# Kernel tuning notes

Hardware: AMD Instinct MI355X
Metric: run time of the kernel (lower is better)

Reference implementation:

```python
import jax, jax.numpy as jnp
import numpy as np

B, S, D_MODEL, D_K = 4, 4096, 1024, 128
NEG = jnp.float32(-1e30)  # acts as -inf for masking; exp underflows to exactly 0 in fp32


def setup_inputs() -> dict:
    key = jax.random.key(0)
    ks = jax.random.split(key, 8)
    sc = 1.0 / np.sqrt(D_MODEL)
    x = jax.random.normal(ks[0], (B, S, D_MODEL), jnp.float32)
    padding_mask = (jax.random.uniform(ks[1], (B, S)) > 0.05).astype(jnp.float32)
    Wq = jax.random.normal(ks[2], (D_MODEL, D_K), jnp.float32) * sc
    bq = jax.random.normal(ks[3], (D_K,), jnp.float32) * 0.01
    Wk = jax.random.normal(ks[4], (D_MODEL, D_K), jnp.float32) * sc
    bk = jax.random.normal(ks[5], (D_K,), jnp.float32) * 0.01
    Wv = jax.random.normal(ks[6], (D_MODEL, D_K), jnp.float32) * sc
    bv = jax.random.normal(ks[7], (D_K,), jnp.float32) * 0.01
    return {"x": x, "padding_mask": padding_mask, "Wq": Wq, "bq": bq,
            "Wk": Wk, "bk": bk, "Wv": Wv, "bv": bv}


def reference(x, padding_mask, Wq, bq, Wk, bk, Wv, bv):
    # Self-attention path (enc_dec_layer_input is None), masked=True (causal).
    scale = jnp.sqrt(jnp.float32(Wq.shape[-1]))
    Q = x @ Wq + bq  # [B,S,Dk]
    K = x @ Wk + bk
    V = x @ Wv + bv
    scores = jnp.einsum('bqd,bkd->bqk', Q, K) / scale  # [B,S,S]
    # causal mask (torch: triu(1) filled with -inf) AND padding outer-product mask
    causal = jnp.tril(jnp.ones((S, S), dtype=bool))  # True = allowed
    pm = (padding_mask[:, :, None] * padding_mask[:, None, :]) > 0  # [B,S,S]
    allowed = causal[None] & pm
    scores = jnp.where(allowed, scores, NEG)
    attn = jax.nn.softmax(scores, axis=-1)
    # torch: fully-masked query rows give NaN -> nan_to_num -> 0.
    # A query row is dead iff its own token is padded (diagonal is causally allowed).
    row_alive = padding_mask > 0  # [B,S]
    attn = jnp.where(row_alive[:, :, None], attn, 0.0)
    out = jnp.einsum('bqk,bkd->bqd', attn, V)  # [B,S,Dk]
    return out
```

## Files before the change

kernel.cpp:

```cpp
#include <hip/hip_runtime.h>
#include <hip/hip_bf16.h>
#include <cstdint>

typedef __bf16 bf16x8 __attribute__((ext_vector_type(8)));
typedef float f32x4 __attribute__((ext_vector_type(4)));

#define MFMA16(a, b, c) __builtin_amdgcn_mfma_f32_16x16x32_bf16((a), (b), (c), 0, 0, 0)

__device__ __forceinline__ unsigned short f2bf(float f) {
  union { float f; unsigned u; } v; v.f = f;
  unsigned u = v.u;
  u += 0x7fffu + ((u >> 16) & 1u);
  return (unsigned short)(u >> 16);
}
__device__ __forceinline__ unsigned pk2(float a, float b) {
  __hip_bfloat162 h = __float22bfloat162_rn(make_float2(a, b));
  union { __hip_bfloat162 h; unsigned u; } v; v.h = h; return v.u;
}

__global__ __launch_bounds__(256) void convert_w(
    const float* __restrict__ Wq, const float* __restrict__ Wk,
    const float* __restrict__ Wv, unsigned short* __restrict__ wt) {
  int idx = blockIdx.x * 256 + threadIdx.x;
  int m = idx >> 17;
  int rem = idx & 131071;
  int k = rem >> 7;
  int n = rem & 127;
  const float* W = (m == 0) ? Wq : (m == 1) ? Wk : Wv;
  wt[(size_t)m * 131072 + (size_t)n * 1024 + k] = f2bf(W[(size_t)k * 128 + n]);
}

__global__ __launch_bounds__(256) void qkv_gemm(
    const float* __restrict__ x, const unsigned short* __restrict__ wt_all,
    const float* __restrict__ bq, const float* __restrict__ bk,
    const float* __restrict__ bv,
    unsigned short* __restrict__ Qg, unsigned short* __restrict__ Kg,
    unsigned short* __restrict__ Vtg) {
  __shared__ unsigned short x_lds[128][40];
  __shared__ unsigned short w_lds[128][40];
  const int tid = threadIdx.x;
  const int lane = tid & 63;
  const int w = tid >> 6;
  const int mode = blockIdx.y;
  const int m0 = blockIdx.x * 128;
  const unsigned short* wt = wt_all + (size_t)mode * 131072;
  const float* bias = (mode == 0) ? bq : (mode == 1) ? bk : bv;

  const int wr = (w >> 1) * 64;
  const int wc = (w & 1) * 64;
  const int lr = lane & 15;
  const int lk = (lane >> 4) * 8;

  f32x4 acc[4][4];
#pragma unroll
  for (int m = 0; m < 4; ++m)
#pragma unroll
    for (int n = 0; n < 4; ++n) acc[m][n] = (f32x4){0.f, 0.f, 0.f, 0.f};

  const int srow = tid >> 1;
  const int shalf = (tid & 1) * 16;
  const float* xrow = x + (size_t)(m0 + srow) * 1024 + shalf;
  const unsigned short* wrow = wt + (size_t)srow * 1024 + shalf;

  float4 xa, xb, xc, xd; uint4 wv0, wv1;
  {
    const float4* s4 = (const float4*)xrow;
    xa = s4[0]; xb = s4[1]; xc = s4[2]; xd = s4[3];
    const uint4* ws4 = (const uint4*)wrow;
    wv0 = ws4[0]; wv1 = ws4[1];
  }

  for (int k0 = 0; k0 < 1024; k0 += 32) {
    __syncthreads();
    {
      uint4 w0, w1;
      w0.x = pk2(xa.x, xa.y);  w0.y = pk2(xa.z, xa.w);
      w0.z = pk2(xb.x, xb.y);  w0.w = pk2(xb.z, xb.w);
      w1.x = pk2(xc.x, xc.y);  w1.y = pk2(xc.z, xc.w);
      w1.z = pk2(xd.x, xd.y);  w1.w = pk2(xd.z, xd.w);
      *(uint4*)&x_lds[srow][shalf] = w0;
      *(uint4*)&x_lds[srow][shalf + 8] = w1;
      *(uint4*)&w_lds[srow][shalf] = wv0;
      *(uint4*)&w_lds[srow][shalf + 8] = wv1;
    }
    __syncthreads();
    if (k0 + 32 < 1024) {
      const float4* s4 = (const float4*)(xrow + k0 + 32);
      xa = s4[0]; xb = s4[1]; xc = s4[2]; xd = s4[3];
      const uint4* ws4 = (const uint4*)(wrow + k0 + 32);
      wv0 = ws4[0]; wv1 = ws4[1];
    }
    bf16x8 af[4], bfr[4];
#pragma unroll
    for (int m = 0; m < 4; ++m) af[m] = *(const bf16x8*)&x_lds[wr + m * 16 + lr][lk];
#pragma unroll
    for (int n = 0; n < 4; ++n) bfr[n] = *(const bf16x8*)&w_lds[wc + n * 16 + lr][lk];
#pragma unroll
    for (int m = 0; m < 4; ++m)
#pragma unroll
      for (int n = 0; n < 4; ++n) acc[m][n] = MFMA16(af[m], bfr[n], acc[m][n]);
  }

  float bcol[4];
#pragma unroll
  for (int n = 0; n < 4; ++n) bcol[n] = bias[wc + n * 16 + lr];
#pragma unroll
  for (int m = 0; m < 4; ++m)
#pragma unroll
    for (int n = 0; n < 4; ++n)
#pragma unroll
      for (int r = 0; r < 4; ++r) {
        int grow = m0 + wr + m * 16 + (lane >> 4) * 4 + r;
        int col = wc + n * 16 + lr;
        float val = acc[m][n][r] + bcol[n];
        if (mode == 0) {
          val *= 0.08838834764831845f;
          Qg[(size_t)grow * 128 + col] = f2bf(val);
        } else if (mode == 1) {
          Kg[(size_t)grow * 128 + col] = f2bf(val);
        } else {
          int bb = grow >> 12, s = grow & 4095;
          Vtg[((size_t)bb * 128 + col) * 4096 + s] = f2bf(val);
        }
      }
}

struct AttnLds {
  unsigned short K_lds[64][136];
  unsigned short V_lds[128][72];
  unsigned short P_lds[4][16][68];
};

__device__ __forceinline__ void attn_tiles(
    AttnLds& S, const unsigned short* __restrict__ Kg,
    const unsigned short* __restrict__ Vtg, const float* __restrict__ pmask,
    int b, int q0, int tstart, int tend,
    const bf16x8 (&qf)[4], float& mrow, float& lsum, f32x4 (&o)[8]) {
  const int tid = threadIdx.x;
  const int lane = tid & 63;
  const int w = tid >> 6;
  const int lr = lane & 15;
  const int lg = lane >> 4;
  const int lk = lg * 8;
  const int q_own = q0 + w * 16 + lr;

  for (int t = tstart; t < tend; ++t) {
    const int k0 = t * 64;
    __syncthreads();
    {
      int kr = tid >> 2, seg = (tid & 3) * 32;
      const uint4* src = (const uint4*)(Kg + ((size_t)b * 4096 + k0 + kr) * 128 + seg);
      uint4 v0 = src[0], v1 = src[1], v2 = src[2], v3 = src[3];
      uint4* dst = (uint4*)&S.K_lds[kr][seg];
      dst[0] = v0; dst[1] = v1; dst[2] = v2; dst[3] = v3;
      int d = tid >> 1, half = (tid & 1) * 32;
      const uint4* vs = (const uint4*)(Vtg + ((size_t)b * 128 + d) * 4096 + k0 + half);
      uint4 u0 = vs[0], u1 = vs[1], u2 = vs[2], u3 = vs[3];
      uint4* vdst = (uint4*)&S.V_lds[d][half];
      vdst[0] = u0; vdst[1] = u1; vdst[2] = u2; vdst[3] = u3;
    }
    __syncthreads();

    f32x4 st[4];
#pragma unroll
    for (int f = 0; f < 4; ++f) {
      st[f] = (f32x4){0.f, 0.f, 0.f, 0.f};
#pragma unroll
      for (int dc = 0; dc < 4; ++dc) {
        bf16x8 kf = *(const bf16x8*)&S.K_lds[f * 16 + lr][dc * 32 + lk];
        st[f] = MFMA16(kf, qf[dc], st[f]);
      }
    }

    const unsigned long long mb = __ballot(pmask[(size_t)b * 4096 + k0 + lane] > 0.f);
    unsigned nib[4];
#pragma unroll
    for (int f = 0; f < 4; ++f) nib[f] = (unsigned)(mb >> (16 * f + 4 * lg)) & 0xFu;

    float mx = -1e30f;
    if (k0 + 63 > q0 + (w << 4)) {
#pragma unroll
      for (int f = 0; f < 4; ++f)
#pragma unroll
        for (int r = 0; r < 4; ++r) {
          const bool ok = (((nib[f] >> r) & 1u) != 0u) &&
                          (k0 + 16 * f + 4 * lg + r <= q_own);
          const float s = ok ? st[f][r] : -1e30f;
          st[f][r] = s;
          mx = fmaxf(mx, s);
        }
    } else {
#pragma unroll
      for (int f = 0; f < 4; ++f)
#pragma unroll
        for (int r = 0; r < 4; ++r) {
          const bool ok = ((nib[f] >> r) & 1u) != 0u;
          const float s = ok ? st[f][r] : -1e30f;
          st[f][r] = s;
          mx = fmaxf(mx, s);
        }
    }
    mx = fmaxf(mx, __shfl_xor(mx, 16));
    mx = fmaxf(mx, __shfl_xor(mx, 32));
    const float mnew = fmaxf(mrow, mx);
    const float alpha = __expf(mrow - mnew);
    mrow = mnew;

    float sum = 0.f;
#pragma unroll
    for (int f = 0; f < 4; ++f) {
      const float p0 = (st[f][0] < -1e29f) ? 0.f : __expf(st[f][0] - mnew);
      const float p1 = (st[f][1] < -1e29f) ? 0.f : __expf(st[f][1] - mnew);
      const float p2 = (st[f][2] < -1e29f) ? 0.f : __expf(st[f][2] - mnew);
      const float p3 = (st[f][3] < -1e29f) ? 0.f : __expf(st[f][3] - mnew);
      sum += (p0 + p1) + (p2 + p3);
      uint2 u; u.x = pk2(p0, p1); u.y = pk2(p2, p3);
      *(uint2*)&S.P_lds[w][lr][16 * f + 4 * lg] = u;
    }
    sum += __shfl_xor(sum, 16);
    sum += __shfl_xor(sum, 32);
    lsum = lsum * alpha + sum;
#pragma unroll
    for (int n = 0; n < 8; ++n) o[n] *= alpha;

    __asm__ volatile("s_waitcnt lgkmcnt(0)" ::: "memory");
#pragma unroll
    for (int kc = 0; kc < 2; ++kc) {
      bf16x8 pa = *(const bf16x8*)&S.P_lds[w][lr][kc * 32 + lk];
#pragma unroll
      for (int n = 0; n < 8; ++n) {
        bf16x8 vf = *(const bf16x8*)&S.V_lds[n * 16 + lr][kc * 32 + lk];
        o[n] = MFMA16(vf, pa, o[n]);
      }
    }
  }
}

__global__ __launch_bounds__(256) void attn_fwd(
    const unsigned short* __restrict__ Qg, const unsigned short* __restrict__ Kg,
    const unsigned short* __restrict__ Vtg, const float* __restrict__ pmask,
    float* __restrict__ out) {
  __shared__ AttnLds S;
  const int tid = threadIdx.x;
  const int lane = tid & 63;
  const int w = tid >> 6;
  const int b = blockIdx.y;
  const int q0 = blockIdx.x * 64;
  const int lr = lane & 15;
  const int lg = lane >> 4;
  const int lk = lg * 8;

  bf16x8 qf[4];
  {
    const unsigned short* qp = Qg + ((size_t)b * 4096 + q0 + w * 16 + lr) * 128;
#pragma unroll
    for (int dc = 0; dc < 4; ++dc) qf[dc] = *(const bf16x8*)(qp + dc * 32 + lk);
  }
  float mrow = -1e30f, lsum = 0.f;
  f32x4 o[8];
#pragma unroll
  for (int n = 0; n < 8; ++n) o[n] = (f32x4){0.f, 0.f, 0.f, 0.f};

  attn_tiles(S, Kg, Vtg, pmask, b, q0, 0, (q0 >> 6) + 1, qf, mrow, lsum, o);

  const int qrow = q0 + w * 16 + lr;
  const bool alive = pmask[(size_t)b * 4096 + qrow] > 0.f;
  const float inv = (alive && lsum > 0.f) ? 1.f / lsum : 0.f;
  float* op = out + ((size_t)b * 4096 + qrow) * 128 + 4 * lg;
#pragma unroll
  for (int n = 0; n < 8; ++n) {
    f32x4 v = o[n] * inv;
    *(f32x4*)(op + n * 16) = v;
  }
}

__global__ __launch_bounds__(256) void attn_split(
    const unsigned short* __restrict__ Qg, const unsigned short* __restrict__ Kg,
    const unsigned short* __restrict__ Vtg, const float* __restrict__ pmask,
    float* __restrict__ out, unsigned short* __restrict__ o_part,
    float* __restrict__ ml_part) {
  __shared__ AttnLds S;
  const int tid = threadIdx.x;
  const int lane = tid & 63;
  const int w = tid >> 6;
  const int L = blockIdx.x;
  const int xcd = L & 7;
  const int b = xcd >> 1;
  const int s = ((L >> 3) << 1) | (xcd & 1);
  int qb, c, nch;
  if (s < 13)       { qb = s;                 c = 0;       nch = 1; }
  else if (s < 39)  { int t = s - 13;  qb = 13 + (t >> 1); c = t & 1;  nch = 2; }
  else if (s < 78)  { int t = s - 39;  qb = 26 + t / 3;    c = t % 3;  nch = 3; }
  else if (s < 130) { int t = s - 78;  qb = 39 + (t >> 2); c = t & 3;  nch = 4; }
  else              { int t = s - 130; qb = 52 + t / 5;    c = t % 5;  nch = 5; }
  const int q0 = qb * 64;
  const int tstart = c * 13;
  const int tend = min(c * 13 + 13, qb + 1);
  const int lr = lane & 15;
  const int lg = lane >> 4;
  const int lk = lg * 8;

  bf16x8 qf[4];
  {
    const unsigned short* qp = Qg + ((size_t)b * 4096 + q0 + w * 16 + lr) * 128;
#pragma unroll
    for (int dc = 0; dc < 4; ++dc) qf[dc] = *(const bf16x8*)(qp + dc * 32 + lk);
  }
  float mrow = -1e30f, lsum = 0.f;
  f32x4 o[8];
#pragma unroll
  for (int n = 0; n < 8; ++n) o[n] = (f32x4){0.f, 0.f, 0.f, 0.f};

  attn_tiles(S, Kg, Vtg, pmask, b, q0, tstart, tend, qf, mrow, lsum, o);

  if (nch == 1) {
    const int qrow = q0 + w * 16 + lr;
    const bool alive = pmask[(size_t)b * 4096 + qrow] > 0.f;
    const float inv = (alive && lsum > 0.f) ? 1.f / lsum : 0.f;
    float* op = out + ((size_t)b * 4096 + qrow) * 128 + 4 * lg;
#pragma unroll
    for (int n = 0; n < 8; ++n) {
      f32x4 v = o[n] * inv;
      *(f32x4*)(op + n * 16) = v;
    }
  } else {
    const int slot = (b * 64 + qb) * 5 + c;
    unsigned short* op = o_part + ((size_t)slot * 64 + w * 16 + lr) * 128 + 4 * lg;
#pragma unroll
    for (int n = 0; n < 8; ++n) {
      uint2 u; u.x = pk2(o[n][0], o[n][1]); u.y = pk2(o[n][2], o[n][3]);
      *(uint2*)(op + n * 16) = u;
    }
    if (lane < 16) {
      float* mp = ml_part + ((size_t)slot * 64 + w * 16 + lane) * 2;
      mp[0] = mrow;
      mp[1] = lsum;
    }
  }
}

__global__ __launch_bounds__(256) void attn_combine(
    const unsigned short* __restrict__ o_part, const float* __restrict__ ml_part,
    const float* __restrict__ pmask, float* __restrict__ out) {
  const int tid = threadIdx.x;
  const int lane = tid & 63;
  const int w = tid >> 6;
  const int g = blockIdx.x * 4 + w;
  const int b = g / 3264;
  const int rem = g % 3264;
  const int qb = 13 + (rem >> 6);
  const int row = rem & 63;
  const int qrow = qb * 64 + row;
  const int nch = (qb + 13) / 13;
  const int pbase = (b * 64 + qb) * 5;

  float m[5], l[5];
  float M = -1e30f;
  for (int c = 0; c < nch; ++c) {
    const float* mp = ml_part + ((size_t)(pbase + c) * 64 + row) * 2;
    m[c] = mp[0];
    l[c] = mp[1];
    M = fmaxf(M, m[c]);
  }
  float L = 0.f, wgt[5];
  for (int c = 0; c < nch; ++c) {
    wgt[c] = __expf(m[c] - M);
    L += wgt[c] * l[c];
  }
  float2 acc = {0.f, 0.f};
  for (int c = 0; c < nch; ++c) {
    const unsigned u = *(const unsigned*)(o_part + ((size_t)(pbase + c) * 64 + row) * 128 + lane * 2);
    acc.x += wgt[c] * __uint_as_float(u << 16);
    acc.y += wgt[c] * __uint_as_float(u & 0xffff0000u);
  }
  const bool alive = pmask[(size_t)b * 4096 + qrow] > 0.f;
  const float inv = (alive && L > 0.f) ? 1.f / L : 0.f;
  float2* op = (float2*)(out + ((size_t)b * 4096 + qrow) * 128);
  op[lane] = make_float2(acc.x * inv, acc.y * inv);
}

extern "C" void kernel_launch(void* const* d_in, const int* in_sizes, int n_in,
                              void* d_out, int out_size, void* d_ws, size_t ws_size,
                              hipStream_t stream) {
  (void)in_sizes; (void)n_in; (void)out_size;
  const float* x  = (const float*)d_in[0];
  const float* pm = (const float*)d_in[1];
  const float* Wq = (const float*)d_in[2];
  const float* bq = (const float*)d_in[3];
  const float* Wk = (const float*)d_in[4];
  const float* bk = (const float*)d_in[5];
  const float* Wv = (const float*)d_in[6];
  const float* bv = (const float*)d_in[7];
  float* out = (float*)d_out;

  unsigned short* ws  = (unsigned short*)d_ws;
  unsigned short* wt  = ws;
  unsigned short* Qg  = ws + 393216;
  unsigned short* Kg  = Qg + 2097152;
  unsigned short* Vtg = Kg + 2097152;
  unsigned short* o_part = ws + 6684672;
  float* ml_part = (float*)(ws + 17170432);
  const size_t WS_NEED = 34996224u;

  convert_w<<<1536, 256, 0, stream>>>(Wq, Wk, Wv, wt);
  qkv_gemm<<<dim3(128, 3), 256, 0, stream>>>(x, wt, bq, bk, bv, Qg, Kg, Vtg);
  if (ws_size >= WS_NEED) {
    attn_split<<<760, 256, 0, stream>>>(Qg, Kg, Vtg, pm, out, o_part, ml_part);
    attn_combine<<<3264, 256, 0, stream>>>(o_part, ml_part, pm, out);
  } else {
    attn_fwd<<<dim3(64, 4), 256, 0, stream>>>(Qg, Kg, Vtg, pm, out);
  }
}
```

Measured before the change: 115.6 us.

## Read V directly from global, shrink split chunks to 8 tiles, raise occupancy

After: 183.0 us. +58.2%, slower.

```diff
diff --git a/kernel.cpp b/kernel.cpp
--- a/kernel.cpp
+++ b/kernel.cpp
@@ -127,14 +127,13 @@
 
 struct AttnLds {
   unsigned short K_lds[64][136];
-  unsigned short V_lds[128][72];
   unsigned short P_lds[4][16][68];
 };
 
 __device__ __forceinline__ void attn_tiles(
-    AttnLds& S, const unsigned short* __restrict__ Kg,
-    const unsigned short* __restrict__ Vtg, const float* __restrict__ pmask,
-    int b, int q0, int tstart, int tend,
+    AttnLds& S, const unsigned short* __restrict__ Kb,
+    const unsigned short* __restrict__ Vb, const float* __restrict__ pmb,
+    int q0, int tstart, int tend,
     const bf16x8 (&qf)[4], float& mrow, float& lsum, f32x4 (&o)[8]) {
   const int tid = threadIdx.x;
   const int lane = tid & 63;
@@ -149,15 +148,10 @@
     __syncthreads();
     {
       int kr = tid >> 2, seg = (tid & 3) * 32;
-      const uint4* src = (const uint4*)(Kg + ((size_t)b * 4096 + k0 + kr) * 128 + seg);
+      const uint4* src = (const uint4*)(Kb + (size_t)(k0 + kr) * 128 + seg);
       uint4 v0 = src[0], v1 = src[1], v2 = src[2], v3 = src[3];
       uint4* dst = (uint4*)&S.K_lds[kr][seg];
       dst[0] = v0; dst[1] = v1; dst[2] = v2; dst[3] = v3;
-      int d = tid >> 1, half = (tid & 1) * 32;
-      const uint4* vs = (const uint4*)(Vtg + ((size_t)b * 128 + d) * 4096 + k0 + half);
-      uint4 u0 = vs[0], u1 = vs[1], u2 = vs[2], u3 = vs[3];
-      uint4* vdst = (uint4*)&S.V_lds[d][half];
-      vdst[0] = u0; vdst[1] = u1; vdst[2] = u2; vdst[3] = u3;
     }
     __syncthreads();
 
@@ -172,7 +166,7 @@
       }
     }
 
-    const unsigned long long mb = __ballot(pmask[(size_t)b * 4096 + k0 + lane] > 0.f);
+    const unsigned long long mb = __ballot(pmb[k0 + lane] > 0.f);
     unsigned nib[4];
 #pragma unroll
     for (int f = 0; f < 4; ++f) nib[f] = (unsigned)(mb >> (16 * f + 4 * lg)) & 0xFu;
@@ -229,14 +223,14 @@
       bf16x8 pa = *(const bf16x8*)&S.P_lds[w][lr][kc * 32 + lk];
 #pragma unroll
       for (int n = 0; n < 8; ++n) {
-        bf16x8 vf = *(const bf16x8*)&S.V_lds[n * 16 + lr][kc * 32 + lk];
+        bf16x8 vf = *(const bf16x8*)(Vb + (size_t)(n * 16 + lr) * 4096 + k0 + kc * 32 + lk);
         o[n] = MFMA16(vf, pa, o[n]);
       }
     }
   }
 }
 
-__global__ __launch_bounds__(256) void attn_fwd(
+__global__ __launch_bounds__(256, 5) void attn_fwd(
     const unsigned short* __restrict__ Qg, const unsigned short* __restrict__ Kg,
     const unsigned short* __restrict__ Vtg, const float* __restrict__ pmask,
     float* __restrict__ out) {
@@ -261,7 +255,8 @@
 #pragma unroll
   for (int n = 0; n < 8; ++n) o[n] = (f32x4){0.f, 0.f, 0.f, 0.f};
 
-  attn_tiles(S, Kg, Vtg, pmask, b, q0, 0, (q0 >> 6) + 1, qf, mrow, lsum, o);
+  attn_tiles(S, Kg + (size_t)b * 4096 * 128, Vtg + (size_t)b * 128 * 4096,
+             pmask + (size_t)b * 4096, q0, 0, (q0 >> 6) + 1, qf, mrow, lsum, o);
 
   const int qrow = q0 + w * 16 + lr;
   const bool alive = pmask[(size_t)b * 4096 + qrow] > 0.f;
@@ -274,7 +269,7 @@
   }
 }
 
-__global__ __launch_bounds__(256) void attn_split(
+__global__ __launch_bounds__(256, 5) void attn_split(
     const unsigned short* __restrict__ Qg, const unsigned short* __restrict__ Kg,
     const unsigned short* __restrict__ Vtg, const float* __restrict__ pmask,
     float* __restrict__ out, unsigned short* __restrict__ o_part,
@@ -288,14 +283,22 @@
   const int b = xcd >> 1;
   const int s = ((L >> 3) << 1) | (xcd & 1);
   int qb, c, nch;
-  if (s < 13)       { qb = s;                 c = 0;       nch = 1; }
-  else if (s < 39)  { int t = s - 13;  qb = 13 + (t >> 1); c = t & 1;  nch = 2; }
-  else if (s < 78)  { int t = s - 39;  qb = 26 + t / 3;    c = t % 3;  nch = 3; }
-  else if (s < 130) { int t = s - 78;  qb = 39 + (t >> 2); c = t & 3;  nch = 4; }
-  else              { int t = s - 130; qb = 52 + t / 5;    c = t % 5;  nch = 5; }
+  if (s < 8) {
+    qb = s; c = 0; nch = 1;
+  } else {
+    int g = 1;
+#pragma unroll
+    for (int gg = 2; gg <= 7; ++gg)
+      if (s >= 4 * gg * (gg + 1)) g = gg;
+    const int rel = s - 4 * g * (g + 1);
+    const int qq = rel / (g + 1);
+    qb = 8 * g + qq;
+    c = rel - qq * (g + 1);
+    nch = g + 1;
+  }
   const int q0 = qb * 64;
-  const int tstart = c * 13;
-  const int tend = min(c * 13 + 13, qb + 1);
+  const int tstart = c * 8;
+  const int tend = min(c * 8 + 8, qb + 1);
   const int lr = lane & 15;
   const int lg = lane >> 4;
   const int lk = lg * 8;
@@ -311,7 +314,8 @@
 #pragma unroll
   for (int n = 0; n < 8; ++n) o[n] = (f32x4){0.f, 0.f, 0.f, 0.f};
 
-  attn_tiles(S, Kg, Vtg, pmask, b, q0, tstart, tend, qf, mrow, lsum, o);
+  attn_tiles(S, Kg + (size_t)b * 4096 * 128, Vtg + (size_t)b * 128 * 4096,
+             pmask + (size_t)b * 4096, q0, tstart, tend, qf, mrow, lsum, o);
 
   if (nch == 1) {
     const int qrow = q0 + w * 16 + lr;
@@ -324,7 +328,7 @@
       *(f32x4*)(op + n * 16) = v;
     }
   } else {
-    const int slot = (b * 64 + qb) * 5 + c;
+    const int slot = b * 280 + (s - 8);
     unsigned short* op = o_part + ((size_t)slot * 64 + w * 16 + lr) * 128 + 4 * lg;
 #pragma unroll
     for (int n = 0; n < 8; ++n) {
@@ -346,33 +350,40 @@
   const int lane = tid & 63;
   const int w = tid >> 6;
   const int g = blockIdx.x * 4 + w;
-  const int b = g / 3264;
-  const int rem = g % 3264;
-  const int qb = 13 + (rem >> 6);
+  const int b = g / 3584;
+  const int rem = g % 3584;
+  const int qb = 8 + (rem >> 6);
   const int row = rem & 63;
   const int qrow = qb * 64 + row;
-  const int nch = (qb + 13) / 13;
-  const int pbase = (b * 64 + qb) * 5;
-
-  float m[5], l[5];
+  const int grp = qb >> 3;
+  const int nch = grp + 1;
+  const int pbase = b * 280 + 4 * grp * (grp + 1) - 8 + (qb - 8 * grp) * nch;
+
+  float m[8], l[8];
   float M = -1e30f;
-  for (int c = 0; c < nch; ++c) {
-    const float* mp = ml_part + ((size_t)(pbase + c) * 64 + row) * 2;
-    m[c] = mp[0];
-    l[c] = mp[1];
-    M = fmaxf(M, m[c]);
-  }
-  float L = 0.f, wgt[5];
-  for (int c = 0; c < nch; ++c) {
-    wgt[c] = __expf(m[c] - M);
-    L += wgt[c] * l[c];
-  }
+#pragma unroll
+  for (int c = 0; c < 8; ++c)
+    if (c < nch) {
+      const float* mp = ml_part + ((size_t)(pbase + c) * 64 + row) * 2;
+      m[c] = mp[0];
+      l[c] = mp[1];
+      M = fmaxf(M, m[c]);
+    }
+  float L = 0.f, wgt[8];
+#pragma unroll
+  for (int c = 0; c < 8; ++c)
+    if (c < nch) {
+      wgt[c] = __expf(m[c] - M);
+      L += wgt[c] * l[c];
+    }
   float2 acc = {0.f, 0.f};
-  for (int c = 0; c < nch; ++c) {
-    const unsigned u = *(const unsigned*)(o_part + ((size_t)(pbase + c) * 64 + row) * 128 + lane * 2);
-    acc.x += wgt[c] * __uint_as_float(u << 16);
-    acc.y += wgt[c] * __uint_as_float(u & 0xffff0000u);
-  }
+#pragma unroll
+  for (int c = 0; c < 8; ++c)
+    if (c < nch) {
+      const unsigned u = *(const unsigned*)(o_part + ((size_t)(pbase + c) * 64 + row) * 128 + lane * 2);
+      acc.x += wgt[c] * __uint_as_float(u << 16);
+      acc.y += wgt[c] * __uint_as_float(u & 0xffff0000u);
+    }
   const bool alive = pmask[(size_t)b * 4096 + qrow] > 0.f;
   const float inv = (alive && L > 0.f) ? 1.f / L : 0.f;
   float2* op = (float2*)(out + ((size_t)b * 4096 + qrow) * 128);
@@ -399,14 +410,14 @@
   unsigned short* Kg  = Qg + 2097152;
   unsigned short* Vtg = Kg + 2097152;
   unsigned short* o_part = ws + 6684672;
-  float* ml_part = (float*)(ws + 17170432);
-  const size_t WS_NEED = 34996224u;
+  float* ml_part = (float*)(ws + 15859712);
+  const size_t WS_NEED = 15859712u * 2u + 573440u;
 
   convert_w<<<1536, 256, 0, stream>>>(Wq, Wk, Wv, wt);
   qkv_gemm<<<dim3(128, 3), 256, 0, stream>>>(x, wt, bq, bk, bv, Qg, Kg, Vtg);
   if (ws_size >= WS_NEED) {
-    attn_split<<<760, 256, 0, stream>>>(Qg, Kg, Vtg, pm, out, o_part, ml_part);
-    attn_combine<<<3264, 256, 0, stream>>>(o_part, ml_part, pm, out);
+    attn_split<<<1152, 256, 0, stream>>>(Qg, Kg, Vtg, pm, out, o_part, ml_part);
+    attn_combine<<<3584, 256, 0, stream>>>(o_part, ml_part, pm, out);
   } else {
     attn_fwd<<<dim3(64, 4), 256, 0, stream>>>(Qg, Kg, Vtg, pm, out);
   }
```
